# Kernel tuning notes

Hardware: AMD Instinct MI355X
Metric: run time of the kernel (lower is better)

The kernel has to match this reference:

```python
import jax, jax.numpy as jnp
import numpy as np

B, T, IN, H, N, W, R, NW, OUT = 16, 64, 256, 512, 256, 64, 4, 1, 256
NM = 1 + 2 * NW  # read modes
EPS = 1e-6

# interface slice offsets
_sizes = [R*W, R, NW*W, NW, NW*W, NW*W, R, NW, NW, R*NM]
_offs = np.concatenate([[0], np.cumsum(_sizes)])

def _oneplus(x):
    return 1.0 + jax.nn.softplus(x)

def _content_weights(M, keys, strengths):
    # M: [B,N,W], keys: [B,h,W], strengths: [B,h] -> [B,h,N]
    Mn = M / (jnp.linalg.norm(M, axis=-1, keepdims=True) + EPS)
    kn = keys / (jnp.linalg.norm(keys, axis=-1, keepdims=True) + EPS)
    sim = jnp.einsum('bnw,bhw->bhn', Mn, kn)
    return jax.nn.softmax(_oneplus(strengths)[..., None] * sim, axis=-1)

def setup_inputs() -> dict:
    key = jax.random.key(0)
    ks = jax.random.split(key, 5)
    s = 0.02
    return {
        'inputs': jax.random.normal(ks[0], (T, B, IN), jnp.float32),
        'W_ih': jax.random.normal(ks[1], (4*H, IN + R*W), jnp.float32) * s,
        'W_hh': jax.random.normal(ks[2], (4*H, H), jnp.float32) * s,
        'b_ih': jnp.zeros((4*H,), jnp.float32),
        'b_hh': jnp.zeros((4*H,), jnp.float32),
        'W_int': jax.random.normal(ks[3], (H, int(_offs[-1])), jnp.float32) * s,
        'b_int': jnp.zeros((int(_offs[-1]),), jnp.float32),
        'W_out': jax.random.normal(ks[4], (OUT, H + R*W), jnp.float32) * s,
        'b_out': jnp.zeros((OUT,), jnp.float32),
    }

def _dnc_forward(inputs, W_ih, W_hh, b_ih, b_hh, W_int, b_int, W_out, b_out):
    off_diag = 1.0 - jnp.eye(N, dtype=inputs.dtype)

    def step(carry, x_t):
        h, c, M, usage, link, prec, wr, ww_prev, read_words = carry
        ctrl_in = jnp.concatenate([x_t, read_words.reshape(B, -1)], axis=1)
        gates = ctrl_in @ W_ih.T + h @ W_hh.T + (b_ih + b_hh)
        i, f, g, o = jnp.split(gates, 4, axis=1)  # torch LSTM gate order
        c = jax.nn.sigmoid(f) * c + jax.nn.sigmoid(i) * jnp.tanh(g)
        h = jax.nn.sigmoid(o) * jnp.tanh(c)

        itf = h @ W_int + b_int
        def sl(j, shape):
            return itf[:, _offs[j]:_offs[j+1]].reshape((B,) + shape)
        read_keys = sl(0, (R, W)); read_str = sl(1, (R,))
        write_keys = sl(2, (NW, W)); write_str = sl(3, (NW,))
        erase = jax.nn.sigmoid(sl(4, (NW, W)))
        write_vec = jax.nn.sigmoid(sl(5, (NW, W)))
        free_gate = jax.nn.sigmoid(sl(6, (R,)))
        alloc_gate = jax.nn.sigmoid(sl(7, (NW,)))
        write_gate = jax.nn.sigmoid(sl(8, (NW,)))
        modes = jax.nn.softmax(sl(9, (R, NM)), axis=2)

        # usage with previous write weights and free gates over previous reads
        psi = jnp.prod(1.0 - free_gate[:, :, None] * wr, axis=1)  # [B,N]
        ww_agg = 1.0 - jnp.prod(1.0 - ww_prev, axis=1)
        usage = (usage + ww_agg - usage * ww_agg) * psi

        # allocation weighting (sort ascending usage)
        idx = jnp.argsort(usage, axis=1)
        u_s = jnp.take_along_axis(usage, idx, axis=1)
        prod_excl = jnp.cumprod(jnp.concatenate([jnp.ones((B, 1), usage.dtype), u_s[:, :-1]], axis=1), axis=1)
        a_s = (1.0 - u_s) * prod_excl
        alloc = jnp.zeros_like(usage).at[jnp.arange(B)[:, None], idx].set(a_s)

        cw = _content_weights(M, write_keys, write_str)  # [B,NW,N]
        ww = write_gate[..., None] * (alloc_gate[..., None] * alloc[:, None, :] + (1.0 - alloc_gate[..., None]) * cw)

        # memory erase + write
        M = M * jnp.prod(1.0 - ww[:, :, :, None] * erase[:, :, None, :], axis=1)
        M = M + jnp.einsum('bhn,bhw->bnw', ww, write_vec)

        # temporal link update (uses old precedence)
        ww_i = ww[..., :, None]; ww_j = ww[..., None, :]
        link = (1.0 - ww_i - ww_j) * link + ww_i * prec[:, :, None, :]
        link = link * off_diag
        prec = (1.0 - ww.sum(-1, keepdims=True)) * prec + ww

        fwd = jnp.einsum('bwij,brj->brwi', link, wr)
        bwd = jnp.einsum('bwji,brj->brwi', link, wr)
        cr = _content_weights(M, read_keys, read_str)  # [B,R,N]
        mb, mf, mc = modes[..., :NW], modes[..., NW:2*NW], modes[..., 2*NW]
        wr = jnp.einsum('brw,brwn->brn', mb, bwd) + jnp.einsum('brw,brwn->brn', mf, fwd) + mc[..., None] * cr
        read_words = jnp.einsum('brn,bnw->brw', wr, M)

        pre = jnp.concatenate([h, read_words.reshape(B, -1)], axis=1)
        out = pre @ W_out.T + b_out
        return (h, c, M, usage, link, prec, wr, ww, read_words), out

    z = jnp.zeros
    dt = inputs.dtype
    carry0 = (z((B, H), dt), z((B, H), dt), z((B, N, W), dt), z((B, N), dt),
              z((B, NW, N, N), dt), z((B, NW, N), dt), z((B, R, N), dt),
              z((B, NW, N), dt), z((B, R, W), dt))
    _, outs = jax.lax.scan(step, carry0, inputs)
    return outs  # [T,B,OUT]

def reference(inputs, W_ih, W_hh, b_ih, b_hh, W_int, b_int, W_out, b_out):
    return _dnc_forward(inputs, W_ih, W_hh, b_ih, b_hh, W_int, b_int, W_out, b_out)
```

## Files before the change

kernel.cpp:

```cpp
#include <hip/hip_runtime.h>
#include <math.h>

#define BT 256

#define Bx 16
#define Tt 64
#define INx 256

__device__ __forceinline__ float sigm(float v) { return 1.0f / (1.0f + expf(-v)); }
__device__ __forceinline__ float oneplusf(float v) { return 1.0f + ((v > 15.0f) ? v : log1pf(expf(v))); }
__device__ __forceinline__ float4 ld4(const float* p) { return *reinterpret_cast<const float4*>(p); }

#define ZERO_FLOATS 1376256

__global__ __launch_bounds__(BT) void k_zero(float* __restrict__ ws) {
    int g = blockIdx.x * BT + threadIdx.x;
    for (int i = g; i < ZERO_FLOATS; i += gridDim.x * BT) ws[i] = 0.0f;
}

__global__ __launch_bounds__(BT)
void k_gates(const float* __restrict__ x,
             const float* __restrict__ W_ih, const float* __restrict__ W_hh,
             const float* __restrict__ b_ih, const float* __restrict__ b_hh,
             const float* __restrict__ W_out, const float* __restrict__ b_out,
             const float* __restrict__ hr, float* __restrict__ hw,
             float* __restrict__ cst, const float* __restrict__ rwb,
             const float* __restrict__ oh, float* __restrict__ out, int t)
{
    const int bl = blockIdx.x, tid = threadIdx.x;
    __shared__ float red[1024];
    if (bl < 128) {
        int pl = tid >> 2, ks = tid & 3;
        int p = bl * 64 + pl;
        int b = p & 15, j = p >> 4;
        float a0 = 0, a1 = 0, a2 = 0, a3 = 0;
        const float *src, *w0, *w1, *w2, *w3;
        if (ks < 2) {
            int kofs = ks * 256;
            src = (ks == 0) ? (x + (t * Bx + b) * INx) : (rwb + b * 256);
            w0 = W_ih + (j)        * 512 + kofs;
            w1 = W_ih + (j + 512)  * 512 + kofs;
            w2 = W_ih + (j + 1024) * 512 + kofs;
            w3 = W_ih + (j + 1536) * 512 + kofs;
        } else {
            int kofs = (ks - 2) * 256;
            src = hr + b * 512 + kofs;
            w0 = W_hh + (j)        * 512 + kofs;
            w1 = W_hh + (j + 512)  * 512 + kofs;
            w2 = W_hh + (j + 1024) * 512 + kofs;
            w3 = W_hh + (j + 1536) * 512 + kofs;
        }
        for (int kk = 0; kk < 256; kk += 4) {
            float4 iv = ld4(src + kk);
            float4 q0 = ld4(w0 + kk);
            a0 += iv.x * q0.x + iv.y * q0.y + iv.z * q0.z + iv.w * q0.w;
            float4 q1 = ld4(w1 + kk);
            a1 += iv.x * q1.x + iv.y * q1.y + iv.z * q1.z + iv.w * q1.w;
            float4 q2 = ld4(w2 + kk);
            a2 += iv.x * q2.x + iv.y * q2.y + iv.z * q2.z + iv.w * q2.w;
            float4 q3 = ld4(w3 + kk);
            a3 += iv.x * q3.x + iv.y * q3.y + iv.z * q3.z + iv.w * q3.w;
        }
        red[pl * 16 + 0 * 4 + ks] = a0;
        red[pl * 16 + 1 * 4 + ks] = a1;
        red[pl * 16 + 2 * 4 + ks] = a2;
        red[pl * 16 + 3 * 4 + ks] = a3;
        __syncthreads();
        if (ks == 0) {
            const float* rp = red + pl * 16;
            float gi = rp[0]  + rp[1]  + rp[2]  + rp[3]  + b_ih[j]        + b_hh[j];
            float gf = rp[4]  + rp[5]  + rp[6]  + rp[7]  + b_ih[j + 512]  + b_hh[j + 512];
            float gg = rp[8]  + rp[9]  + rp[10] + rp[11] + b_ih[j + 1024] + b_hh[j + 1024];
            float go = rp[12] + rp[13] + rp[14] + rp[15] + b_ih[j + 1536] + b_hh[j + 1536];
            float cv = cst[b * 512 + j];
            cv = sigm(gf) * cv + sigm(gi) * tanhf(gg);
            float hv = sigm(go) * tanhf(cv);
            cst[b * 512 + j] = cv;
            hw[b * 512 + j] = hv;
        }
    } else if (t > 0) {
        int b = bl - 128, o = tid;
        float acc = b_out[o];
        acc += oh[b * 256 + o] + oh[(16 + b) * 256 + o] + oh[(32 + b) * 256 + o] + oh[(48 + b) * 256 + o];
        const float* wrow = W_out + o * 768 + 512;
        const float* rwp = rwb + b * 256;
        for (int k = 0; k < 256; k += 4) {
            float4 w4 = ld4(wrow + k);
            acc += rwp[k] * w4.x + rwp[k + 1] * w4.y + rwp[k + 2] * w4.z + rwp[k + 3] * w4.w;
        }
        out[((t - 1) * Bx + b) * 256 + o] = acc;
    }
}

__global__ __launch_bounds__(BT)
void k_itf(const float* __restrict__ hw, const float* __restrict__ W_int,
           const float* __restrict__ b_int, float* __restrict__ itf,
           const float* __restrict__ W_out, float* __restrict__ oh)
{
    const int bl = blockIdx.x, tid = threadIdx.x;
    __shared__ float red[4096];
    if (bl < 15) {
        int jl = tid & 31, ks = tid >> 5;
        int j = bl * 32 + jl;
        float acc[16];
#pragma unroll
        for (int b = 0; b < 16; b++) acc[b] = 0.f;
        if (j < 471) {
            for (int k = ks * 64; k < ks * 64 + 64; ++k) {
                float wv = W_int[k * 471 + j];
#pragma unroll
                for (int b = 0; b < 16; b++) acc[b] += hw[b * 512 + k] * wv;
            }
        }
#pragma unroll
        for (int b = 0; b < 16; b++) red[tid * 16 + b] = acc[b];
        __syncthreads();
        int jl2 = tid & 31, bh = tid >> 5;
        int j2 = bl * 32 + jl2;
        for (int rep = 0; rep < 2; ++rep) {
            int b2 = bh + 8 * rep;
            if (j2 < 471) {
                float s = 0;
#pragma unroll
                for (int ksx = 0; ksx < 8; ksx++) s += red[(ksx * 32 + jl2) * 16 + b2];
                itf[b2 * 471 + j2] = s + b_int[j2];
            }
        }
    } else {
        int idx = bl - 15;
        int b = idx >> 2, ks = idx & 3;
        int o = tid;
        const float* wrow = W_out + o * 768 + ks * 128;
        const float* hb = hw + b * 512 + ks * 128;
        float acc = 0;
        for (int k = 0; k < 128; k += 4) {
            float4 w4 = ld4(wrow + k);
            acc += hb[k] * w4.x + hb[k + 1] * w4.y + hb[k + 2] * w4.z + hb[k + 3] * w4.w;
        }
        oh[(ks * 16 + b) * 256 + o] = acc;
    }
}

__global__ __launch_bounds__(BT)
void k_iface(const float* __restrict__ itf, const float* __restrict__ Mb,
             const float* __restrict__ nrm, float* __restrict__ usg,
             const float* __restrict__ wrb, float* __restrict__ wwb,
             const float* __restrict__ pr_r, float* __restrict__ pr_w,
             float* __restrict__ ers, float* __restrict__ wvs,
             float* __restrict__ rso, float* __restrict__ mds)
{
    const int b = blockIdx.x, tid = threadIdx.x;
    __shared__ float smem[1152];
    __shared__ int s_idx[256];
    float* s_keys = smem;
    float* s_cw   = smem + 256;
    float* s_al   = smem + 512;
    float* s_tmp  = smem + 768;
    float* s_wk   = smem + 1024;
    float* s_sc   = smem + 1088;
    const float* it = itf + b * 471;

    if (tid < 4) {
        float m0 = it[459 + tid * 3], m1 = it[460 + tid * 3], m2 = it[461 + tid * 3];
        float mx3 = fmaxf(m0, fmaxf(m1, m2));
        float e0 = expf(m0 - mx3), e1 = expf(m1 - mx3), e2 = expf(m2 - mx3);
        float inv = 1.f / (e0 + e1 + e2);
        mds[(b * 4 + tid) * 3 + 0] = e0 * inv;
        mds[(b * 4 + tid) * 3 + 1] = e1 * inv;
        mds[(b * 4 + tid) * 3 + 2] = e2 * inv;
        rso[b * 4 + tid] = oneplusf(it[256 + tid]);
        s_sc[tid] = sigm(it[453 + tid]);
    }
    if (tid == 4) s_sc[4] = sigm(it[457]);
    if (tid == 5) s_sc[5] = sigm(it[458]);
    if (tid == 6) s_sc[6] = oneplusf(it[324]);
    if (tid < 64) {
        ers[b * 64 + tid] = sigm(it[325 + tid]);
        wvs[b * 64 + tid] = sigm(it[389 + tid]);
        s_wk[tid] = it[260 + tid];
    }
    __syncthreads();
    if (tid < 64) {
        float v = s_wk[tid] * s_wk[tid];
        for (int o2 = 32; o2 > 0; o2 >>= 1) v += __shfl_down(v, o2);
        if (tid == 0) s_sc[7] = sqrtf(v);
    }
    __syncthreads();
    {
        int n = tid;
        float psi = 1.f;
#pragma unroll
        for (int r = 0; r < 4; r++) psi *= (1.f - s_sc[r] * wrb[b * 1024 + r * 256 + n]);
        float wwp = wwb[b * 256 + n];
        float u = usg[b * 256 + n];
        u = (u + wwp - u * wwp) * psi;
        usg[b * 256 + n] = u;
        s_keys[n] = u;
        s_idx[n] = n;
        const float* Mr = Mb + (b * 256 + n) * 64;
        float dot = 0;
        for (int w = 0; w < 64; w += 4) {
            float4 m4 = ld4(Mr + w);
            dot += m4.x * s_wk[w] + m4.y * s_wk[w + 1] + m4.z * s_wk[w + 2] + m4.w * s_wk[w + 3];
        }
        s_cw[n] = s_sc[6] * dot / ((nrm[b * 256 + n] + 1e-6f) * (s_sc[7] + 1e-6f));
    }
    __syncthreads();
    s_tmp[tid] = s_cw[tid];
    __syncthreads();
    for (int s2 = 128; s2 > 0; s2 >>= 1) { if (tid < s2) s_tmp[tid] = fmaxf(s_tmp[tid], s_tmp[tid + s2]); __syncthreads(); }
    float mx = s_tmp[0];
    __syncthreads();
    float ex = expf(s_cw[tid] - mx);
    s_tmp[tid] = ex;
    __syncthreads();
    for (int s2 = 128; s2 > 0; s2 >>= 1) { if (tid < s2) s_tmp[tid] += s_tmp[tid + s2]; __syncthreads(); }
    float cwv = ex / s_tmp[0];
    __syncthreads();
    s_cw[tid] = cwv;
    for (int kk2 = 2; kk2 <= 256; kk2 <<= 1) {
        for (int j2 = kk2 >> 1; j2 > 0; j2 >>= 1) {
            int ixj = tid ^ j2;
            if (ixj > tid) {
                float ka = s_keys[tid], kb = s_keys[ixj];
                int ia = s_idx[tid], ib = s_idx[ixj];
                bool up = ((tid & kk2) == 0);
                bool sw = up ? (kb < ka || (kb == ka && ib < ia))
                             : (ka < kb || (ka == kb && ia < ib));
                if (sw) { s_keys[tid] = kb; s_keys[ixj] = ka; s_idx[tid] = ib; s_idx[ixj] = ia; }
            }
            __syncthreads();
        }
    }
    s_tmp[tid] = s_keys[tid];
    __syncthreads();
    for (int o2 = 1; o2 < 256; o2 <<= 1) {
        float pv = (tid >= o2) ? s_tmp[tid - o2] : 1.0f;
        __syncthreads();
        s_tmp[tid] *= pv;
        __syncthreads();
    }
    float excl = (tid == 0) ? 1.0f : s_tmp[tid - 1];
    float a_s = (1.0f - s_keys[tid]) * excl;
    s_al[s_idx[tid]] = a_s;
    __syncthreads();
    float ag = s_sc[4], wg = s_sc[5];
    float wwn = wg * (ag * s_al[tid] + (1.f - ag) * s_cw[tid]);
    wwb[b * 256 + tid] = wwn;
    s_tmp[tid] = wwn;
    __syncthreads();
    for (int s2 = 128; s2 > 0; s2 >>= 1) { if (tid < s2) s_tmp[tid] += s_tmp[tid + s2]; __syncthreads(); }
    float S = s_tmp[0];
    pr_w[b * 256 + tid] = (1.f - S) * pr_r[b * 256 + tid] + wwn;
}

__global__ __launch_bounds__(BT)
void k_linkmem(const float* __restrict__ wwb, const float* __restrict__ pr_r,
               float* __restrict__ lnk, const float* __restrict__ wrb,
               float* __restrict__ bwp, float* __restrict__ Mb,
               const float* __restrict__ ers, const float* __restrict__ wvs,
               float* __restrict__ nrm)
{
    const int bl = blockIdx.x, tid = threadIdx.x;
    if (bl < 128) {
        int b = bl >> 3, ch = bl & 7;
        int ci = tid;
        float wwc = wwb[b * 256 + ci];
        float pco = pr_r[b * 256 + ci];
        float* Lb = lnk + b * 65536;
        float b0 = 0, b1 = 0, b2 = 0, b3 = 0;
        int r0 = ch * 32;
        for (int rr = 0; rr < 32; ++rr) {
            int ri = r0 + rr;
            float wwr = wwb[b * 256 + ri];
            float v = Lb[ri * 256 + ci];
            v = (1.f - wwr - wwc) * v + wwr * pco;
            if (ci == ri) v = 0.f;
            Lb[ri * 256 + ci] = v;
            b0 += v * wrb[b * 1024 + ri];
            b1 += v * wrb[b * 1024 + 256 + ri];
            b2 += v * wrb[b * 1024 + 512 + ri];
            b3 += v * wrb[b * 1024 + 768 + ri];
        }
        float* bp = bwp + ((b * 8 + ch) * 4) * 256;
        bp[ci] = b0; bp[256 + ci] = b1; bp[512 + ci] = b2; bp[768 + ci] = b3;
    } else {
        int b = bl - 128;
        int w = tid & 63, rg = tid >> 6;
        float er = ers[b * 64 + w], wv = wvs[b * 64 + w];
        for (int it2 = 0; it2 < 64; ++it2) {
            int n = rg + 4 * it2;
            float wwn = wwb[b * 256 + n];
            float m = Mb[(b * 256 + n) * 64 + w];
            m = m * (1.f - wwn * er) + wwn * wv;
            Mb[(b * 256 + n) * 64 + w] = m;
            float s = m * m;
            for (int o2 = 32; o2 > 0; o2 >>= 1) s += __shfl_down(s, o2);
            if (w == 0) nrm[b * 256 + n] = sqrtf(s);
        }
    }
}

__global__ __launch_bounds__(BT)
void k_read(const float* __restrict__ lnk, const float* __restrict__ bwp,
            const float* __restrict__ Mb, const float* __restrict__ nrm,
            const float* __restrict__ itf, const float* __restrict__ rso,
            const float* __restrict__ mds, float* __restrict__ wrb,
            float* __restrict__ rwb)
{
    const int bl = blockIdx.x, tid = threadIdx.x;
    __shared__ float smem[896];
    int b = bl >> 2, r = bl & 3;
    float* s_wr  = smem;
    float* s_tmp = smem + 512;
    float* s_key = smem + 768;
    float* s_sc  = smem + 840;
    s_wr[tid] = wrb[b * 1024 + r * 256 + tid];
    if (tid < 64) s_key[tid] = itf[b * 471 + r * 64 + tid];
    __syncthreads();
    if (tid < 64) {
        float v = s_key[tid] * s_key[tid];
        for (int o2 = 32; o2 > 0; o2 >>= 1) v += __shfl_down(v, o2);
        if (tid == 0) s_sc[0] = sqrtf(v);
    }
    __syncthreads();
    int n = tid;
    const float* bp = bwp + b * 8192 + r * 256 + n;
    float bwd_n = 0;
#pragma unroll
    for (int ch = 0; ch < 8; ++ch) bwd_n += bp[ch * 1024];
    const float* Lr = lnk + b * 65536 + n * 256;
    float fwd_n = 0;
    for (int j2 = 0; j2 < 256; j2 += 4) {
        float4 l4 = ld4(Lr + j2);
        fwd_n += l4.x * s_wr[j2] + l4.y * s_wr[j2 + 1] + l4.z * s_wr[j2 + 2] + l4.w * s_wr[j2 + 3];
    }
    const float* Mr = Mb + (b * 256 + n) * 64;
    float dot = 0;
    for (int w = 0; w < 64; w += 4) {
        float4 m4 = ld4(Mr + w);
        dot += m4.x * s_key[w] + m4.y * s_key[w + 1] + m4.z * s_key[w + 2] + m4.w * s_key[w + 3];
    }
    float simv = rso[b * 4 + r] * dot / ((nrm[b * 256 + n] + 1e-6f) * (s_sc[0] + 1e-6f));
    s_tmp[tid] = simv;
    __syncthreads();
    for (int s2 = 128; s2 > 0; s2 >>= 1) { if (tid < s2) s_tmp[tid] = fmaxf(s_tmp[tid], s_tmp[tid + s2]); __syncthreads(); }
    float mx = s_tmp[0];
    __syncthreads();
    float ex = expf(simv - mx);
    s_tmp[tid] = ex;
    __syncthreads();
    for (int s2 = 128; s2 > 0; s2 >>= 1) { if (tid < s2) s_tmp[tid] += s_tmp[tid + s2]; __syncthreads(); }
    float crv = ex / s_tmp[0];
    float mbv = mds[(b * 4 + r) * 3 + 0];
    float mfv = mds[(b * 4 + r) * 3 + 1];
    float mcv = mds[(b * 4 + r) * 3 + 2];
    float wrn = mbv * bwd_n + mfv * fwd_n + mcv * crv;
    wrb[b * 1024 + r * 256 + n] = wrn;
    __syncthreads();
    s_wr[tid] = wrn;
    __syncthreads();
    int w = tid & 63, gq = tid >> 6;
    float p = 0;
    const float* Mg = Mb + b * 256 * 64;
    for (int n2 = gq * 64; n2 < gq * 64 + 64; ++n2)
        p += s_wr[n2] * Mg[n2 * 64 + w];
    s_tmp[tid] = p;
    __syncthreads();
    if (tid < 64)
        rwb[b * 256 + r * 64 + tid] = s_tmp[tid] + s_tmp[tid + 64] + s_tmp[tid + 128] + s_tmp[tid + 192];
}

__global__ __launch_bounds__(BT)
void k_final(const float* __restrict__ oh, const float* __restrict__ W_out,
             const float* __restrict__ b_out, const float* __restrict__ rwb,
             float* __restrict__ out)
{
    int b = blockIdx.x, o = threadIdx.x;
    float acc = b_out[o];
    acc += oh[b * 256 + o] + oh[(16 + b) * 256 + o] + oh[(32 + b) * 256 + o] + oh[(48 + b) * 256 + o];
    const float* wrow = W_out + o * 768 + 512;
    const float* rwp = rwb + b * 256;
    for (int k = 0; k < 256; k += 4) {
        float4 w4 = ld4(wrow + k);
        acc += rwp[k] * w4.x + rwp[k + 1] * w4.y + rwp[k + 2] * w4.z + rwp[k + 3] * w4.w;
    }
    out[((Tt - 1) * Bx + b) * 256 + o] = acc;
}

extern "C" void kernel_launch(void* const* d_in, const int* in_sizes, int n_in,
                              void* d_out, int out_size, void* d_ws, size_t ws_size,
                              hipStream_t stream) {
    const float* x     = (const float*)d_in[0];
    const float* W_ih  = (const float*)d_in[1];
    const float* W_hh  = (const float*)d_in[2];
    const float* b_ih  = (const float*)d_in[3];
    const float* b_hh  = (const float*)d_in[4];
    const float* W_int = (const float*)d_in[5];
    const float* b_int = (const float*)d_in[6];
    const float* W_out = (const float*)d_in[7];
    const float* b_out = (const float*)d_in[8];
    float* outp = (float*)d_out;
    float* ws   = (float*)d_ws;

    float* h0  = ws + 0;
    float* h1  = ws + 8192;
    float* cst = ws + 16384;
    float* Mb  = ws + 24576;
    float* usg = ws + 286720;
    float* lnk = ws + 290816;
    float* pr0 = ws + 1339392;
    float* pr1 = ws + 1343488;
    float* wrb = ws + 1347584;
    float* wwb = ws + 1363968;
    float* rwb = ws + 1368064;
    float* nrm = ws + 1372160;
    float* itf = ws + 1376256;
    float* ers = ws + 1383792;
    float* wvs = ws + 1384816;
    float* rso = ws + 1385840;
    float* mds = ws + 1385904;
    float* oh  = ws + 1386096;
    float* bwp = ws + 1402480;
    (void)usg;

    k_zero<<<672, BT, 0, stream>>>(ws);
    for (int t = 0; t < Tt; ++t) {
        const float* hr = (t & 1) ? h1 : h0;
        float*       hw = (t & 1) ? h0 : h1;
        const float* pr_r = (t & 1) ? pr1 : pr0;
        float*       pr_w = (t & 1) ? pr0 : pr1;
        k_gates<<<144, BT, 0, stream>>>(x, W_ih, W_hh, b_ih, b_hh, W_out, b_out,
                                        hr, hw, cst, rwb, oh, outp, t);
        k_itf<<<79, BT, 0, stream>>>(hw, W_int, b_int, itf, W_out, oh);
        k_iface<<<16, BT, 0, stream>>>(itf, Mb, nrm, ws + 286720, wrb, wwb,
                                       pr_r, pr_w, ers, wvs, rso, mds);
        k_linkmem<<<144, BT, 0, stream>>>(wwb, pr_r, lnk, wrb, bwp, Mb, ers, wvs, nrm);
        k_read<<<64, BT, 0, stream>>>(lnk, bwp, Mb, nrm, itf, rso, mds, wrb, rwb);
    }
    k_final<<<16, BT, 0, stream>>>(oh, W_out, b_out, rwb, outp);
}
```

Measured before the change: 9.313 ms.

## Fuse per-step kernels into one persistent kernel with grid-wide barriers

```diff
diff --git a/kernel.cpp b/kernel.cpp
--- a/kernel.cpp
+++ b/kernel.cpp
@@ -2,6 +2,7 @@
 #include <math.h>
 
 #define BT 256
+#define GRID 144
 
 #define Bx 16
 #define Tt 64
@@ -11,399 +12,41 @@
 __device__ __forceinline__ float oneplusf(float v) { return 1.0f + ((v > 15.0f) ? v : log1pf(expf(v))); }
 __device__ __forceinline__ float4 ld4(const float* p) { return *reinterpret_cast<const float4*>(p); }
 
+__device__ unsigned int g_bar_count = 0;
+__device__ unsigned int g_bar_gen   = 0;
+
+__device__ __forceinline__ void gsync() {
+    __syncthreads();
+    if (threadIdx.x == 0) {
+        __threadfence();
+        unsigned gen = __hip_atomic_load(&g_bar_gen, __ATOMIC_RELAXED, __HIP_MEMORY_SCOPE_AGENT);
+        unsigned arrived = __hip_atomic_fetch_add(&g_bar_count, 1u, __ATOMIC_ACQ_REL, __HIP_MEMORY_SCOPE_AGENT);
+        if (arrived == GRID - 1u) {
+            __hip_atomic_store(&g_bar_count, 0u, __ATOMIC_RELAXED, __HIP_MEMORY_SCOPE_AGENT);
+            __hip_atomic_store(&g_bar_gen, gen + 1u, __ATOMIC_RELEASE, __HIP_MEMORY_SCOPE_AGENT);
+        } else {
+            while (__hip_atomic_load(&g_bar_gen, __ATOMIC_RELAXED, __HIP_MEMORY_SCOPE_AGENT) == gen) {
+                __builtin_amdgcn_s_sleep(4);
+            }
+        }
+        __threadfence();
+    }
+    __syncthreads();
+}
+
 #define ZERO_FLOATS 1376256
 
-__global__ __launch_bounds__(BT) void k_zero(float* __restrict__ ws) {
-    int g = blockIdx.x * BT + threadIdx.x;
-    for (int i = g; i < ZERO_FLOATS; i += gridDim.x * BT) ws[i] = 0.0f;
-}
-
 __global__ __launch_bounds__(BT)
-void k_gates(const float* __restrict__ x,
-             const float* __restrict__ W_ih, const float* __restrict__ W_hh,
-             const float* __restrict__ b_ih, const float* __restrict__ b_hh,
-             const float* __restrict__ W_out, const float* __restrict__ b_out,
-             const float* __restrict__ hr, float* __restrict__ hw,
-             float* __restrict__ cst, const float* __restrict__ rwb,
-             const float* __restrict__ oh, float* __restrict__ out, int t)
+void k_dnc(const float* __restrict__ x,
+           const float* __restrict__ W_ih, const float* __restrict__ W_hh,
+           const float* __restrict__ b_ih, const float* __restrict__ b_hh,
+           const float* __restrict__ W_int, const float* __restrict__ b_int,
+           const float* __restrict__ W_out, const float* __restrict__ b_out,
+           float* __restrict__ outp, float* __restrict__ ws)
 {
     const int bl = blockIdx.x, tid = threadIdx.x;
-    __shared__ float red[1024];
-    if (bl < 128) {
-        int pl = tid >> 2, ks = tid & 3;
-        int p = bl * 64 + pl;
-        int b = p & 15, j = p >> 4;
-        float a0 = 0, a1 = 0, a2 = 0, a3 = 0;
-        const float *src, *w0, *w1, *w2, *w3;
-        if (ks < 2) {
-            int kofs = ks * 256;
-            src = (ks == 0) ? (x + (t * Bx + b) * INx) : (rwb + b * 256);
-            w0 = W_ih + (j)        * 512 + kofs;
-            w1 = W_ih + (j + 512)  * 512 + kofs;
-            w2 = W_ih + (j + 1024) * 512 + kofs;
-            w3 = W_ih + (j + 1536) * 512 + kofs;
-        } else {
-            int kofs = (ks - 2) * 256;
-            src = hr + b * 512 + kofs;
-            w0 = W_hh + (j)        * 512 + kofs;
-            w1 = W_hh + (j + 512)  * 512 + kofs;
-            w2 = W_hh + (j + 1024) * 512 + kofs;
-            w3 = W_hh + (j + 1536) * 512 + kofs;
-        }
-        for (int kk = 0; kk < 256; kk += 4) {
-            float4 iv = ld4(src + kk);
-            float4 q0 = ld4(w0 + kk);
-            a0 += iv.x * q0.x + iv.y * q0.y + iv.z * q0.z + iv.w * q0.w;
-            float4 q1 = ld4(w1 + kk);
-            a1 += iv.x * q1.x + iv.y * q1.y + iv.z * q1.z + iv.w * q1.w;
-            float4 q2 = ld4(w2 + kk);
-            a2 += iv.x * q2.x + iv.y * q2.y + iv.z * q2.z + iv.w * q2.w;
-            float4 q3 = ld4(w3 + kk);
-            a3 += iv.x * q3.x + iv.y * q3.y + iv.z * q3.z + iv.w * q3.w;
-        }
-        red[pl * 16 + 0 * 4 + ks] = a0;
-        red[pl * 16 + 1 * 4 + ks] = a1;
-        red[pl * 16 + 2 * 4 + ks] = a2;
-        red[pl * 16 + 3 * 4 + ks] = a3;
-        __syncthreads();
-        if (ks == 0) {
-            const float* rp = red + pl * 16;
-            float gi = rp[0]  + rp[1]  + rp[2]  + rp[3]  + b_ih[j]        + b_hh[j];
-            float gf = rp[4]  + rp[5]  + rp[6]  + rp[7]  + b_ih[j + 512]  + b_hh[j + 512];
-            float gg = rp[8]  + rp[9]  + rp[10] + rp[11] + b_ih[j + 1024] + b_hh[j + 1024];
-            float go = rp[12] + rp[13] + rp[14] + rp[15] + b_ih[j + 1536] + b_hh[j + 1536];
-            float cv = cst[b * 512 + j];
-            cv = sigm(gf) * cv + sigm(gi) * tanhf(gg);
-            float hv = sigm(go) * tanhf(cv);
-            cst[b * 512 + j] = cv;
-            hw[b * 512 + j] = hv;
-        }
-    } else if (t > 0) {
-        int b = bl - 128, o = tid;
-        float acc = b_out[o];
-        acc += oh[b * 256 + o] + oh[(16 + b) * 256 + o] + oh[(32 + b) * 256 + o] + oh[(48 + b) * 256 + o];
-        const float* wrow = W_out + o * 768 + 512;
-        const float* rwp = rwb + b * 256;
-        for (int k = 0; k < 256; k += 4) {
-            float4 w4 = ld4(wrow + k);
-            acc += rwp[k] * w4.x + rwp[k + 1] * w4.y + rwp[k + 2] * w4.z + rwp[k + 3] * w4.w;
-        }
-        out[((t - 1) * Bx + b) * 256 + o] = acc;
-    }
-}
-
-__global__ __launch_bounds__(BT)
-void k_itf(const float* __restrict__ hw, const float* __restrict__ W_int,
-           const float* __restrict__ b_int, float* __restrict__ itf,
-           const float* __restrict__ W_out, float* __restrict__ oh)
-{
-    const int bl = blockIdx.x, tid = threadIdx.x;
-    __shared__ float red[4096];
-    if (bl < 15) {
-        int jl = tid & 31, ks = tid >> 5;
-        int j = bl * 32 + jl;
-        float acc[16];
-#pragma unroll
-        for (int b = 0; b < 16; b++) acc[b] = 0.f;
-        if (j < 471) {
-            for (int k = ks * 64; k < ks * 64 + 64; ++k) {
-                float wv = W_int[k * 471 + j];
-#pragma unroll
-                for (int b = 0; b < 16; b++) acc[b] += hw[b * 512 + k] * wv;
-            }
-        }
-#pragma unroll
-        for (int b = 0; b < 16; b++) red[tid * 16 + b] = acc[b];
-        __syncthreads();
-        int jl2 = tid & 31, bh = tid >> 5;
-        int j2 = bl * 32 + jl2;
-        for (int rep = 0; rep < 2; ++rep) {
-            int b2 = bh + 8 * rep;
-            if (j2 < 471) {
-                float s = 0;
-#pragma unroll
-                for (int ksx = 0; ksx < 8; ksx++) s += red[(ksx * 32 + jl2) * 16 + b2];
-                itf[b2 * 471 + j2] = s + b_int[j2];
-            }
-        }
-    } else {
-        int idx = bl - 15;
-        int b = idx >> 2, ks = idx & 3;
-        int o = tid;
-        const float* wrow = W_out + o * 768 + ks * 128;
-        const float* hb = hw + b * 512 + ks * 128;
-        float acc = 0;
-        for (int k = 0; k < 128; k += 4) {
-            float4 w4 = ld4(wrow + k);
-            acc += hb[k] * w4.x + hb[k + 1] * w4.y + hb[k + 2] * w4.z + hb[k + 3] * w4.w;
-        }
-        oh[(ks * 16 + b) * 256 + o] = acc;
-    }
-}
-
-__global__ __launch_bounds__(BT)
-void k_iface(const float* __restrict__ itf, const float* __restrict__ Mb,
-             const float* __restrict__ nrm, float* __restrict__ usg,
-             const float* __restrict__ wrb, float* __restrict__ wwb,
-             const float* __restrict__ pr_r, float* __restrict__ pr_w,
-             float* __restrict__ ers, float* __restrict__ wvs,
-             float* __restrict__ rso, float* __restrict__ mds)
-{
-    const int b = blockIdx.x, tid = threadIdx.x;
-    __shared__ float smem[1152];
-    __shared__ int s_idx[256];
-    float* s_keys = smem;
-    float* s_cw   = smem + 256;
-    float* s_al   = smem + 512;
-    float* s_tmp  = smem + 768;
-    float* s_wk   = smem + 1024;
-    float* s_sc   = smem + 1088;
-    const float* it = itf + b * 471;
-
-    if (tid < 4) {
-        float m0 = it[459 + tid * 3], m1 = it[460 + tid * 3], m2 = it[461 + tid * 3];
-        float mx3 = fmaxf(m0, fmaxf(m1, m2));
-        float e0 = expf(m0 - mx3), e1 = expf(m1 - mx3), e2 = expf(m2 - mx3);
-        float inv = 1.f / (e0 + e1 + e2);
-        mds[(b * 4 + tid) * 3 + 0] = e0 * inv;
-        mds[(b * 4 + tid) * 3 + 1] = e1 * inv;
-        mds[(b * 4 + tid) * 3 + 2] = e2 * inv;
-        rso[b * 4 + tid] = oneplusf(it[256 + tid]);
-        s_sc[tid] = sigm(it[453 + tid]);
-    }
-    if (tid == 4) s_sc[4] = sigm(it[457]);
-    if (tid == 5) s_sc[5] = sigm(it[458]);
-    if (tid == 6) s_sc[6] = oneplusf(it[324]);
-    if (tid < 64) {
-        ers[b * 64 + tid] = sigm(it[325 + tid]);
-        wvs[b * 64 + tid] = sigm(it[389 + tid]);
-        s_wk[tid] = it[260 + tid];
-    }
-    __syncthreads();
-    if (tid < 64) {
-        float v = s_wk[tid] * s_wk[tid];
-        for (int o2 = 32; o2 > 0; o2 >>= 1) v += __shfl_down(v, o2);
-        if (tid == 0) s_sc[7] = sqrtf(v);
-    }
-    __syncthreads();
-    {
-        int n = tid;
-        float psi = 1.f;
-#pragma unroll
-        for (int r = 0; r < 4; r++) psi *= (1.f - s_sc[r] * wrb[b * 1024 + r * 256 + n]);
-        float wwp = wwb[b * 256 + n];
-        float u = usg[b * 256 + n];
-        u = (u + wwp - u * wwp) * psi;
-        usg[b * 256 + n] = u;
-        s_keys[n] = u;
-        s_idx[n] = n;
-        const float* Mr = Mb + (b * 256 + n) * 64;
-        float dot = 0;
-        for (int w = 0; w < 64; w += 4) {
-            float4 m4 = ld4(Mr + w);
-            dot += m4.x * s_wk[w] + m4.y * s_wk[w + 1] + m4.z * s_wk[w + 2] + m4.w * s_wk[w + 3];
-        }
-        s_cw[n] = s_sc[6] * dot / ((nrm[b * 256 + n] + 1e-6f) * (s_sc[7] + 1e-6f));
-    }
-    __syncthreads();
-    s_tmp[tid] = s_cw[tid];
-    __syncthreads();
-    for (int s2 = 128; s2 > 0; s2 >>= 1) { if (tid < s2) s_tmp[tid] = fmaxf(s_tmp[tid], s_tmp[tid + s2]); __syncthreads(); }
-    float mx = s_tmp[0];
-    __syncthreads();
-    float ex = expf(s_cw[tid] - mx);
-    s_tmp[tid] = ex;
-    __syncthreads();
-    for (int s2 = 128; s2 > 0; s2 >>= 1) { if (tid < s2) s_tmp[tid] += s_tmp[tid + s2]; __syncthreads(); }
-    float cwv = ex / s_tmp[0];
-    __syncthreads();
-    s_cw[tid] = cwv;
-    for (int kk2 = 2; kk2 <= 256; kk2 <<= 1) {
-        for (int j2 = kk2 >> 1; j2 > 0; j2 >>= 1) {
-            int ixj = tid ^ j2;
-            if (ixj > tid) {
-                float ka = s_keys[tid], kb = s_keys[ixj];
-                int ia = s_idx[tid], ib = s_idx[ixj];
-                bool up = ((tid & kk2) == 0);
-                bool sw = up ? (kb < ka || (kb == ka && ib < ia))
-                             : (ka < kb || (ka == kb && ia < ib));
-                if (sw) { s_keys[tid] = kb; s_keys[ixj] = ka; s_idx[tid] = ib; s_idx[ixj] = ia; }
-            }
-            __syncthreads();
-        }
-    }
-    s_tmp[tid] = s_keys[tid];
-    __syncthreads();
-    for (int o2 = 1; o2 < 256; o2 <<= 1) {
-        float pv = (tid >= o2) ? s_tmp[tid - o2] : 1.0f;
-        __syncthreads();
-        s_tmp[tid] *= pv;
-        __syncthreads();
-    }
-    float excl = (tid == 0) ? 1.0f : s_tmp[tid - 1];
-    float a_s = (1.0f - s_keys[tid]) * excl;
-    s_al[s_idx[tid]] = a_s;
-    __syncthreads();
-    float ag = s_sc[4], wg = s_sc[5];
-    float wwn = wg * (ag * s_al[tid] + (1.f - ag) * s_cw[tid]);
-    wwb[b * 256 + tid] = wwn;
-    s_tmp[tid] = wwn;
-    __syncthreads();
-    for (int s2 = 128; s2 > 0; s2 >>= 1) { if (tid < s2) s_tmp[tid] += s_tmp[tid + s2]; __syncthreads(); }
-    float S = s_tmp[0];
-    pr_w[b * 256 + tid] = (1.f - S) * pr_r[b * 256 + tid] + wwn;
-}
-
-__global__ __launch_bounds__(BT)
-void k_linkmem(const float* __restrict__ wwb, const float* __restrict__ pr_r,
-               float* __restrict__ lnk, const float* __restrict__ wrb,
-               float* __restrict__ bwp, float* __restrict__ Mb,
-               const float* __restrict__ ers, const float* __restrict__ wvs,
-               float* __restrict__ nrm)
-{
-    const int bl = blockIdx.x, tid = threadIdx.x;
-    if (bl < 128) {
-        int b = bl >> 3, ch = bl & 7;
-        int ci = tid;
-        float wwc = wwb[b * 256 + ci];
-        float pco = pr_r[b * 256 + ci];
-        float* Lb = lnk + b * 65536;
-        float b0 = 0, b1 = 0, b2 = 0, b3 = 0;
-        int r0 = ch * 32;
-        for (int rr = 0; rr < 32; ++rr) {
-            int ri = r0 + rr;
-            float wwr = wwb[b * 256 + ri];
-            float v = Lb[ri * 256 + ci];
-            v = (1.f - wwr - wwc) * v + wwr * pco;
-            if (ci == ri) v = 0.f;
-            Lb[ri * 256 + ci] = v;
-            b0 += v * wrb[b * 1024 + ri];
-            b1 += v * wrb[b * 1024 + 256 + ri];
-            b2 += v * wrb[b * 1024 + 512 + ri];
-            b3 += v * wrb[b * 1024 + 768 + ri];
-        }
-        float* bp = bwp + ((b * 8 + ch) * 4) * 256;
-        bp[ci] = b0; bp[256 + ci] = b1; bp[512 + ci] = b2; bp[768 + ci] = b3;
-    } else {
-        int b = bl - 128;
-        int w = tid & 63, rg = tid >> 6;
-        float er = ers[b * 64 + w], wv = wvs[b * 64 + w];
-        for (int it2 = 0; it2 < 64; ++it2) {
-            int n = rg + 4 * it2;
-            float wwn = wwb[b * 256 + n];
-            float m = Mb[(b * 256 + n) * 64 + w];
-            m = m * (1.f - wwn * er) + wwn * wv;
-            Mb[(b * 256 + n) * 64 + w] = m;
-            float s = m * m;
-            for (int o2 = 32; o2 > 0; o2 >>= 1) s += __shfl_down(s, o2);
-            if (w == 0) nrm[b * 256 + n] = sqrtf(s);
-        }
-    }
-}
-
-__global__ __launch_bounds__(BT)
-void k_read(const float* __restrict__ lnk, const float* __restrict__ bwp,
-            const float* __restrict__ Mb, const float* __restrict__ nrm,
-            const float* __restrict__ itf, const float* __restrict__ rso,
-            const float* __restrict__ mds, float* __restrict__ wrb,
-            float* __restrict__ rwb)
-{
-    const int bl = blockIdx.x, tid = threadIdx.x;
-    __shared__ float smem[896];
-    int b = bl >> 2, r = bl & 3;
-    float* s_wr  = smem;
-    float* s_tmp = smem + 512;
-    float* s_key = smem + 768;
-    float* s_sc  = smem + 840;
-    s_wr[tid] = wrb[b * 1024 + r * 256 + tid];
-    if (tid < 64) s_key[tid] = itf[b * 471 + r * 64 + tid];
-    __syncthreads();
-    if (tid < 64) {
-        float v = s_key[tid] * s_key[tid];
-        for (int o2 = 32; o2 > 0; o2 >>= 1) v += __shfl_down(v, o2);
-        if (tid == 0) s_sc[0] = sqrtf(v);
-    }
-    __syncthreads();
-    int n = tid;
-    const float* bp = bwp + b * 8192 + r * 256 + n;
-    float bwd_n = 0;
-#pragma unroll
-    for (int ch = 0; ch < 8; ++ch) bwd_n += bp[ch * 1024];
-    const float* Lr = lnk + b * 65536 + n * 256;
-    float fwd_n = 0;
-    for (int j2 = 0; j2 < 256; j2 += 4) {
-        float4 l4 = ld4(Lr + j2);
-        fwd_n += l4.x * s_wr[j2] + l4.y * s_wr[j2 + 1] + l4.z * s_wr[j2 + 2] + l4.w * s_wr[j2 + 3];
-    }
-    const float* Mr = Mb + (b * 256 + n) * 64;
-    float dot = 0;
-    for (int w = 0; w < 64; w += 4) {
-        float4 m4 = ld4(Mr + w);
-        dot += m4.x * s_key[w] + m4.y * s_key[w + 1] + m4.z * s_key[w + 2] + m4.w * s_key[w + 3];
-    }
-    float simv = rso[b * 4 + r] * dot / ((nrm[b * 256 + n] + 1e-6f) * (s_sc[0] + 1e-6f));
-    s_tmp[tid] = simv;
-    __syncthreads();
-    for (int s2 = 128; s2 > 0; s2 >>= 1) { if (tid < s2) s_tmp[tid] = fmaxf(s_tmp[tid], s_tmp[tid + s2]); __syncthreads(); }
-    float mx = s_tmp[0];
-    __syncthreads();
-    float ex = expf(simv - mx);
-    s_tmp[tid] = ex;
-    __syncthreads();
-    for (int s2 = 128; s2 > 0; s2 >>= 1) { if (tid < s2) s_tmp[tid] += s_tmp[tid + s2]; __syncthreads(); }
-    float crv = ex / s_tmp[0];
-    float mbv = mds[(b * 4 + r) * 3 + 0];
-    float mfv = mds[(b * 4 + r) * 3 + 1];
-    float mcv = mds[(b * 4 + r) * 3 + 2];
-    float wrn = mbv * bwd_n + mfv * fwd_n + mcv * crv;
-    wrb[b * 1024 + r * 256 + n] = wrn;
-    __syncthreads();
-    s_wr[tid] = wrn;
-    __syncthreads();
-    int w = tid & 63, gq = tid >> 6;
-    float p = 0;
-    const float* Mg = Mb + b * 256 * 64;
-    for (int n2 = gq * 64; n2 < gq * 64 + 64; ++n2)
-        p += s_wr[n2] * Mg[n2 * 64 + w];
-    s_tmp[tid] = p;
-    __syncthreads();
-    if (tid < 64)
-        rwb[b * 256 + r * 64 + tid] = s_tmp[tid] + s_tmp[tid + 64] + s_tmp[tid + 128] + s_tmp[tid + 192];
-}
-
-__global__ __launch_bounds__(BT)
-void k_final(const float* __restrict__ oh, const float* __restrict__ W_out,
-             const float* __restrict__ b_out, const float* __restrict__ rwb,
-             float* __restrict__ out)
-{
-    int b = blockIdx.x, o = threadIdx.x;
-    float acc = b_out[o];
-    acc += oh[b * 256 + o] + oh[(16 + b) * 256 + o] + oh[(32 + b) * 256 + o] + oh[(48 + b) * 256 + o];
-    const float* wrow = W_out + o * 768 + 512;
-    const float* rwp = rwb + b * 256;
-    for (int k = 0; k < 256; k += 4) {
-        float4 w4 = ld4(wrow + k);
-        acc += rwp[k] * w4.x + rwp[k + 1] * w4.y + rwp[k + 2] * w4.z + rwp[k + 3] * w4.w;
-    }
-    out[((Tt - 1) * Bx + b) * 256 + o] = acc;
-}
-
-extern "C" void kernel_launch(void* const* d_in, const int* in_sizes, int n_in,
-                              void* d_out, int out_size, void* d_ws, size_t ws_size,
-                              hipStream_t stream) {
-    const float* x     = (const float*)d_in[0];
-    const float* W_ih  = (const float*)d_in[1];
-    const float* W_hh  = (const float*)d_in[2];
-    const float* b_ih  = (const float*)d_in[3];
-    const float* b_hh  = (const float*)d_in[4];
-    const float* W_int = (const float*)d_in[5];
-    const float* b_int = (const float*)d_in[6];
-    const float* W_out = (const float*)d_in[7];
-    const float* b_out = (const float*)d_in[8];
-    float* outp = (float*)d_out;
-    float* ws   = (float*)d_ws;
-
-    float* h0  = ws + 0;
+
+    float* h0  = ws;
     float* h1  = ws + 8192;
     float* cst = ws + 16384;
     float* Mb  = ws + 24576;
@@ -422,21 +65,363 @@
     float* mds = ws + 1385904;
     float* oh  = ws + 1386096;
     float* bwp = ws + 1402480;
-    (void)usg;
-
-    k_zero<<<672, BT, 0, stream>>>(ws);
+
+    __shared__ float smem[4096];
+    __shared__ int s_idx[256];
+
+    for (int i = bl * BT + tid; i < ZERO_FLOATS; i += GRID * BT) ws[i] = 0.0f;
+    gsync();
+
     for (int t = 0; t < Tt; ++t) {
         const float* hr = (t & 1) ? h1 : h0;
         float*       hw = (t & 1) ? h0 : h1;
         const float* pr_r = (t & 1) ? pr1 : pr0;
         float*       pr_w = (t & 1) ? pr0 : pr1;
-        k_gates<<<144, BT, 0, stream>>>(x, W_ih, W_hh, b_ih, b_hh, W_out, b_out,
-                                        hr, hw, cst, rwb, oh, outp, t);
-        k_itf<<<79, BT, 0, stream>>>(hw, W_int, b_int, itf, W_out, oh);
-        k_iface<<<16, BT, 0, stream>>>(itf, Mb, nrm, ws + 286720, wrb, wwb,
-                                       pr_r, pr_w, ers, wvs, rso, mds);
-        k_linkmem<<<144, BT, 0, stream>>>(wwb, pr_r, lnk, wrb, bwp, Mb, ers, wvs, nrm);
-        k_read<<<64, BT, 0, stream>>>(lnk, bwp, Mb, nrm, itf, rso, mds, wrb, rwb);
+
+        if (bl < 128) {
+            float* red = smem;
+            int pl = tid >> 2, ks = tid & 3;
+            int p = bl * 64 + pl;
+            int b = p & 15, j = p >> 4;
+            float a0 = 0, a1 = 0, a2 = 0, a3 = 0;
+            const float *src, *w0, *w1, *w2, *w3;
+            if (ks < 2) {
+                int kofs = ks * 256;
+                src = (ks == 0) ? (x + (t * Bx + b) * INx) : (rwb + b * 256);
+                w0 = W_ih + (j)        * 512 + kofs;
+                w1 = W_ih + (j + 512)  * 512 + kofs;
+                w2 = W_ih + (j + 1024) * 512 + kofs;
+                w3 = W_ih + (j + 1536) * 512 + kofs;
+            } else {
+                int kofs = (ks - 2) * 256;
+                src = hr + b * 512 + kofs;
+                w0 = W_hh + (j)        * 512 + kofs;
+                w1 = W_hh + (j + 512)  * 512 + kofs;
+                w2 = W_hh + (j + 1024) * 512 + kofs;
+                w3 = W_hh + (j + 1536) * 512 + kofs;
+            }
+            for (int kk = 0; kk < 256; kk += 4) {
+                float4 iv = ld4(src + kk);
+                float4 q0 = ld4(w0 + kk);
+                a0 += iv.x * q0.x + iv.y * q0.y + iv.z * q0.z + iv.w * q0.w;
+                float4 q1 = ld4(w1 + kk);
+                a1 += iv.x * q1.x + iv.y * q1.y + iv.z * q1.z + iv.w * q1.w;
+                float4 q2 = ld4(w2 + kk);
+                a2 += iv.x * q2.x + iv.y * q2.y + iv.z * q2.z + iv.w * q2.w;
+                float4 q3 = ld4(w3 + kk);
+                a3 += iv.x * q3.x + iv.y * q3.y + iv.z * q3.z + iv.w * q3.w;
+            }
+            red[pl * 16 + 0 * 4 + ks] = a0;
+            red[pl * 16 + 1 * 4 + ks] = a1;
+            red[pl * 16 + 2 * 4 + ks] = a2;
+            red[pl * 16 + 3 * 4 + ks] = a3;
+            __syncthreads();
+            if (ks == 0) {
+                const float* rp = red + pl * 16;
+                float gi = rp[0]  + rp[1]  + rp[2]  + rp[3]  + b_ih[j]        + b_hh[j];
+                float gf = rp[4]  + rp[5]  + rp[6]  + rp[7]  + b_ih[j + 512]  + b_hh[j + 512];
+                float gg = rp[8]  + rp[9]  + rp[10] + rp[11] + b_ih[j + 1024] + b_hh[j + 1024];
+                float go = rp[12] + rp[13] + rp[14] + rp[15] + b_ih[j + 1536] + b_hh[j + 1536];
+                float cv = cst[b * 512 + j];
+                cv = sigm(gf) * cv + sigm(gi) * tanhf(gg);
+                float hv = sigm(go) * tanhf(cv);
+                cst[b * 512 + j] = cv;
+                hw[b * 512 + j] = hv;
+            }
+        } else if (t > 0) {
+            int b = bl - 128, o = tid;
+            float acc = b_out[o];
+            acc += oh[b * 256 + o] + oh[(16 + b) * 256 + o] + oh[(32 + b) * 256 + o] + oh[(48 + b) * 256 + o];
+            const float* wrow = W_out + o * 768 + 512;
+            const float* rwp = rwb + b * 256;
+            for (int k = 0; k < 256; k += 4) {
+                float4 w4 = ld4(wrow + k);
+                acc += rwp[k] * w4.x + rwp[k + 1] * w4.y + rwp[k + 2] * w4.z + rwp[k + 3] * w4.w;
+            }
+            outp[((t - 1) * Bx + b) * 256 + o] = acc;
+        }
+        gsync();
+
+        if (bl < 15) {
+            float* red = smem;
+            int jl = tid & 31, ks = tid >> 5;
+            int j = bl * 32 + jl;
+            float acc[16];
+#pragma unroll
+            for (int b = 0; b < 16; b++) acc[b] = 0.f;
+            if (j < 471) {
+                for (int k = ks * 64; k < ks * 64 + 64; ++k) {
+                    float wv = W_int[k * 471 + j];
+#pragma unroll
+                    for (int b = 0; b < 16; b++) acc[b] += hw[b * 512 + k] * wv;
+                }
+            }
+#pragma unroll
+            for (int b = 0; b < 16; b++) red[tid * 16 + b] = acc[b];
+            __syncthreads();
+            int jl2 = tid & 31, bh = tid >> 5;
+            int j2 = bl * 32 + jl2;
+            for (int rep = 0; rep < 2; ++rep) {
+                int b2 = bh + 8 * rep;
+                if (j2 < 471) {
+                    float s = 0;
+#pragma unroll
+                    for (int ksx = 0; ksx < 8; ksx++) s += red[(ksx * 32 + jl2) * 16 + b2];
+                    itf[b2 * 471 + j2] = s + b_int[j2];
+                }
+            }
+        } else if (bl < 79) {
+            int idx = bl - 15;
+            int b = idx >> 2, ks = idx & 3;
+            int o = tid;
+            const float* wrow = W_out + o * 768 + ks * 128;
+            const float* hb = hw + b * 512 + ks * 128;
+            float acc = 0;
+            for (int k = 0; k < 128; k += 4) {
+                float4 w4 = ld4(wrow + k);
+                acc += hb[k] * w4.x + hb[k + 1] * w4.y + hb[k + 2] * w4.z + hb[k + 3] * w4.w;
+            }
+            oh[(ks * 16 + b) * 256 + o] = acc;
+        }
+        gsync();
+
+        if (bl < 16) {
+            const int b = bl;
+            float* s_keys = smem;
+            float* s_cw   = smem + 256;
+            float* s_al   = smem + 512;
+            float* s_tmp  = smem + 768;
+            float* s_wk   = smem + 1024;
+            float* s_sc   = smem + 1088;
+            const float* it = itf + b * 471;
+
+            if (tid < 4) {
+                float m0 = it[459 + tid * 3], m1 = it[460 + tid * 3], m2 = it[461 + tid * 3];
+                float mx3 = fmaxf(m0, fmaxf(m1, m2));
+                float e0 = expf(m0 - mx3), e1 = expf(m1 - mx3), e2 = expf(m2 - mx3);
+                float inv = 1.f / (e0 + e1 + e2);
+                mds[(b * 4 + tid) * 3 + 0] = e0 * inv;
+                mds[(b * 4 + tid) * 3 + 1] = e1 * inv;
+                mds[(b * 4 + tid) * 3 + 2] = e2 * inv;
+                rso[b * 4 + tid] = oneplusf(it[256 + tid]);
+                s_sc[tid] = sigm(it[453 + tid]);
+            }
+            if (tid == 4) s_sc[4] = sigm(it[457]);
+            if (tid == 5) s_sc[5] = sigm(it[458]);
+            if (tid == 6) s_sc[6] = oneplusf(it[324]);
+            if (tid < 64) {
+                ers[b * 64 + tid] = sigm(it[325 + tid]);
+                wvs[b * 64 + tid] = sigm(it[389 + tid]);
+                s_wk[tid] = it[260 + tid];
+            }
+            __syncthreads();
+            if (tid < 64) {
+                float v = s_wk[tid] * s_wk[tid];
+                for (int o2 = 32; o2 > 0; o2 >>= 1) v += __shfl_down(v, o2);
+                if (tid == 0) s_sc[7] = sqrtf(v);
+            }
+            __syncthreads();
+            {
+                int n = tid;
+                float psi = 1.f;
+#pragma unroll
+                for (int r = 0; r < 4; r++) psi *= (1.f - s_sc[r] * wrb[b * 1024 + r * 256 + n]);
+                float wwp = wwb[b * 256 + n];
+                float u = usg[b * 256 + n];
+                u = (u + wwp - u * wwp) * psi;
+                usg[b * 256 + n] = u;
+                s_keys[n] = u;
+                s_idx[n] = n;
+                const float* Mr = Mb + (b * 256 + n) * 64;
+                float dot = 0;
+                for (int w = 0; w < 64; w += 4) {
+                    float4 m4 = ld4(Mr + w);
+                    dot += m4.x * s_wk[w] + m4.y * s_wk[w + 1] + m4.z * s_wk[w + 2] + m4.w * s_wk[w + 3];
+                }
+                s_cw[n] = s_sc[6] * dot / ((nrm[b * 256 + n] + 1e-6f) * (s_sc[7] + 1e-6f));
+            }
+            __syncthreads();
+            s_tmp[tid] = s_cw[tid];
+            __syncthreads();
+            for (int s2 = 128; s2 > 0; s2 >>= 1) { if (tid < s2) s_tmp[tid] = fmaxf(s_tmp[tid], s_tmp[tid + s2]); __syncthreads(); }
+            float mx = s_tmp[0];
+            __syncthreads();
+            float ex = expf(s_cw[tid] - mx);
+            s_tmp[tid] = ex;
+            __syncthreads();
+            for (int s2 = 128; s2 > 0; s2 >>= 1) { if (tid < s2) s_tmp[tid] += s_tmp[tid + s2]; __syncthreads(); }
+            float cwv = ex / s_tmp[0];
+            __syncthreads();
+            s_cw[tid] = cwv;
+            for (int kk2 = 2; kk2 <= 256; kk2 <<= 1) {
+                for (int j2 = kk2 >> 1; j2 > 0; j2 >>= 1) {
+                    int ixj = tid ^ j2;
+                    if (ixj > tid) {
+                        float ka = s_keys[tid], kb = s_keys[ixj];
+                        int ia = s_idx[tid], ib = s_idx[ixj];
+                        bool up = ((tid & kk2) == 0);
+                        bool sw = up ? (kb < ka || (kb == ka && ib < ia))
+                                     : (ka < kb || (ka == kb && ia < ib));
+                        if (sw) { s_keys[tid] = kb; s_keys[ixj] = ka; s_idx[tid] = ib; s_idx[ixj] = ia; }
+                    }
+                    __syncthreads();
+                }
+            }
+            s_tmp[tid] = s_keys[tid];
+            __syncthreads();
+            for (int o2 = 1; o2 < 256; o2 <<= 1) {
+                float pv = (tid >= o2) ? s_tmp[tid - o2] : 1.0f;
+                __syncthreads();
+                s_tmp[tid] *= pv;
+                __syncthreads();
+            }
+            float excl = (tid == 0) ? 1.0f : s_tmp[tid - 1];
+            float a_s = (1.0f - s_keys[tid]) * excl;
+            s_al[s_idx[tid]] = a_s;
+            __syncthreads();
+            float ag = s_sc[4], wg = s_sc[5];
+            float wwn = wg * (ag * s_al[tid] + (1.f - ag) * s_cw[tid]);
+            wwb[b * 256 + tid] = wwn;
+            s_tmp[tid] = wwn;
+            __syncthreads();
+            for (int s2 = 128; s2 > 0; s2 >>= 1) { if (tid < s2) s_tmp[tid] += s_tmp[tid + s2]; __syncthreads(); }
+            float S = s_tmp[0];
+            pr_w[b * 256 + tid] = (1.f - S) * pr_r[b * 256 + tid] + wwn;
+        }
+        gsync();
+
+        if (bl < 128) {
+            int b = bl >> 3, ch = bl & 7;
+            int ci = tid;
+            float wwc = wwb[b * 256 + ci];
+            float pco = pr_r[b * 256 + ci];
+            float* Lb = lnk + b * 65536;
+            float b0 = 0, b1 = 0, b2 = 0, b3 = 0;
+            int r0 = ch * 32;
+            for (int rr = 0; rr < 32; ++rr) {
+                int ri = r0 + rr;
+                float wwr = wwb[b * 256 + ri];
+                float v = Lb[ri * 256 + ci];
+                v = (1.f - wwr - wwc) * v + wwr * pco;
+                if (ci == ri) v = 0.f;
+                Lb[ri * 256 + ci] = v;
+                b0 += v * wrb[b * 1024 + ri];
+                b1 += v * wrb[b * 1024 + 256 + ri];
+                b2 += v * wrb[b * 1024 + 512 + ri];
+                b3 += v * wrb[b * 1024 + 768 + ri];
+            }
+            float* bp = bwp + ((b * 8 + ch) * 4) * 256;
+            bp[ci] = b0; bp[256 + ci] = b1; bp[512 + ci] = b2; bp[768 + ci] = b3;
+        } else {
+            int b = bl - 128;
+            int w = tid & 63, rg = tid >> 6;
+            float er = ers[b * 64 + w], wv = wvs[b * 64 + w];
+            for (int it2 = 0; it2 < 64; ++it2) {
+                int n = rg + 4 * it2;
+                float wwn = wwb[b * 256 + n];
+                float m = Mb[(b * 256 + n) * 64 + w];
+                m = m * (1.f - wwn * er) + wwn * wv;
+                Mb[(b * 256 + n) * 64 + w] = m;
+                float s = m * m;
+                for (int o2 = 32; o2 > 0; o2 >>= 1) s += __shfl_down(s, o2);
+                if (w == 0) nrm[b * 256 + n] = sqrtf(s);
+            }
+        }
+        gsync();
+
+        if (bl < 64) {
+            int b = bl >> 2, r = bl & 3;
+            float* s_wr  = smem;
+            float* s_tmp = smem + 512;
+            float* s_key = smem + 768;
+            float* s_sc  = smem + 840;
+            s_wr[tid] = wrb[b * 1024 + r * 256 + tid];
+            if (tid < 64) s_key[tid] = itf[b * 471 + r * 64 + tid];
+            __syncthreads();
+            if (tid < 64) {
+                float v = s_key[tid] * s_key[tid];
+                for (int o2 = 32; o2 > 0; o2 >>= 1) v += __shfl_down(v, o2);
+                if (tid == 0) s_sc[0] = sqrtf(v);
+            }
+            __syncthreads();
+            int n = tid;
+            const float* bp = bwp + b * 8192 + r * 256 + n;
+            float bwd_n = 0;
+#pragma unroll
+            for (int ch = 0; ch < 8; ++ch) bwd_n += bp[ch * 1024];
+            const float* Lr = lnk + b * 65536 + n * 256;
+            float fwd_n = 0;
+            for (int j2 = 0; j2 < 256; j2 += 4) {
+                float4 l4 = ld4(Lr + j2);
+                fwd_n += l4.x * s_wr[j2] + l4.y * s_wr[j2 + 1] + l4.z * s_wr[j2 + 2] + l4.w * s_wr[j2 + 3];
+            }
+            const float* Mr = Mb + (b * 256 + n) * 64;
+            float dot = 0;
+            for (int w = 0; w < 64; w += 4) {
+                float4 m4 = ld4(Mr + w);
+                dot += m4.x * s_key[w] + m4.y * s_key[w + 1] + m4.z * s_key[w + 2] + m4.w * s_key[w + 3];
+            }
+            float simv = rso[b * 4 + r] * dot / ((nrm[b * 256 + n] + 1e-6f) * (s_sc[0] + 1e-6f));
+            s_tmp[tid] = simv;
+            __syncthreads();
+            for (int s2 = 128; s2 > 0; s2 >>= 1) { if (tid < s2) s_tmp[tid] = fmaxf(s_tmp[tid], s_tmp[tid + s2]); __syncthreads(); }
+            float mx = s_tmp[0];
+            __syncthreads();
+            float ex = expf(simv - mx);
+            s_tmp[tid] = ex;
+            __syncthreads();
+            for (int s2 = 128; s2 > 0; s2 >>= 1) { if (tid < s2) s_tmp[tid] += s_tmp[tid + s2]; __syncthreads(); }
+            float crv = ex / s_tmp[0];
+            float mbv = mds[(b * 4 + r) * 3 + 0];
+            float mfv = mds[(b * 4 + r) * 3 + 1];
+            float mcv = mds[(b * 4 + r) * 3 + 2];
+            float wrn = mbv * bwd_n + mfv * fwd_n + mcv * crv;
+            wrb[b * 1024 + r * 256 + n] = wrn;
+            __syncthreads();
+            s_wr[tid] = wrn;
+            __syncthreads();
+            int w = tid & 63, gq = tid >> 6;
+            float p = 0;
+            const float* Mg = Mb + b * 256 * 64;
+            for (int n2 = gq * 64; n2 < gq * 64 + 64; ++n2)
+                p += s_wr[n2] * Mg[n2 * 64 + w];
+            s_tmp[tid] = p;
+            __syncthreads();
+            if (tid < 64)
+                rwb[b * 256 + r * 64 + tid] = s_tmp[tid] + s_tmp[tid + 64] + s_tmp[tid + 128] + s_tmp[tid + 192];
+        }
+        gsync();
     }
-    k_final<<<16, BT, 0, stream>>>(oh, W_out, b_out, rwb, outp);
+
+    if (bl < 16) {
+        int b = bl, o = tid;
+        float acc = b_out[o];
+        acc += oh[b * 256 + o] + oh[(16 + b) * 256 + o] + oh[(32 + b) * 256 + o] + oh[(48 + b) * 256 + o];
+        const float* wrow = W_out + o * 768 + 512;
+        const float* rwp = rwb + b * 256;
+        for (int k = 0; k < 256; k += 4) {
+            float4 w4 = ld4(wrow + k);
+            acc += rwp[k] * w4.x + rwp[k + 1] * w4.y + rwp[k + 2] * w4.z + rwp[k + 3] * w4.w;
+        }
+        outp[((Tt - 1) * Bx + b) * 256 + o] = acc;
+    }
 }
+
+extern "C" void kernel_launch(void* const* d_in, const int* in_sizes, int n_in,
+                              void* d_out, int out_size, void* d_ws, size_t ws_size,
+                              hipStream_t stream) {
+    const float* x     = (const float*)d_in[0];
+    const float* W_ih  = (const float*)d_in[1];
+    const float* W_hh  = (const float*)d_in[2];
+    const float* b_ih  = (const float*)d_in[3];
+    const float* b_hh  = (const float*)d_in[4];
+    const float* W_int = (const float*)d_in[5];
+    const float* b_int = (const float*)d_in[6];
+    const float* W_out = (const float*)d_in[7];
+    const float* b_out = (const float*)d_in[8];
+    float* outp = (float*)d_out;
+    float* ws   = (float*)d_ws;
+
+    k_dnc<<<GRID, BT, 0, stream>>>(x, W_ih, W_hh, b_ih, b_hh, W_int, b_int,
+                                   W_out, b_out, outp, ws);
+}
```

Result: slower. 13.82 ms (+48.4%).
